# Kernel tuning notes

Hardware: AMD Instinct MI355X
Metric: run time of the kernel (lower is better)

The kernel has to match this reference:

```python
import jax, jax.numpy as jnp
import numpy as np

B, S, T = 512, 1024, 64


def setup_inputs() -> dict:
    key = jax.random.key(0)
    k1, k2, k3, k4, k5 = jax.random.split(key, 5)
    emissions = jax.random.normal(k1, (B, S, T), dtype=jnp.float32)
    tags = jax.random.randint(k2, (B, S), 0, T, dtype=jnp.int32)
    mask = jnp.ones((B, S), dtype=jnp.float32)
    start_transitions = jax.random.uniform(k3, (T,), minval=-0.1, maxval=0.1, dtype=jnp.float32)
    end_transitions = jax.random.uniform(k4, (T,), minval=-0.1, maxval=0.1, dtype=jnp.float32)
    transitions = jax.random.uniform(k5, (T, T), minval=-0.1, maxval=0.1, dtype=jnp.float32)
    return {"emissions": emissions, "mask": mask, "start_transitions": start_transitions,
            "end_transitions": end_transitions, "transitions": transitions, "tags": tags}


def _log_partition(emissions, mask, start_transitions, end_transitions, transitions):
    # forward-algorithm recurrence over time via lax.scan
    log_alpha0 = start_transitions + emissions[:, 0]  # [B, T]

    def step(log_alpha, xs):
        emit_t, mask_t = xs  # [B, T], [B]
        # [B, T_prev, T_next] -> logsumexp over previous tag
        score_t = log_alpha[:, :, None] + transitions[None, :, :] + emit_t[:, None, :]
        new_log_alpha = jax.nn.logsumexp(score_t, axis=1)
        log_alpha = jnp.where(mask_t[:, None] > 0, new_log_alpha, log_alpha)
        return log_alpha, None

    xs = (jnp.swapaxes(emissions[:, 1:], 0, 1), jnp.swapaxes(mask[:, 1:], 0, 1))
    log_alpha, _ = jax.lax.scan(step, log_alpha0, xs)
    log_alpha = log_alpha + end_transitions
    return jax.nn.logsumexp(log_alpha, axis=1).sum()


def _gold_score(emissions, tags, mask, start_transitions, end_transitions, transitions):
    tag0 = tags[:, 0]
    score = start_transitions[tag0] + jnp.take_along_axis(emissions[:, 0], tag0[:, None], axis=1)[:, 0]
    # vectorized over t = 1..S-1
    emit_t = jnp.take_along_axis(emissions[:, 1:], tags[:, 1:, None], axis=2)[..., 0]  # [B, S-1]
    trans_t = transitions[tags[:, :-1], tags[:, 1:]]  # [B, S-1]
    score = score + ((emit_t + trans_t) * mask[:, 1:]).sum(axis=1)
    last_idx = mask.sum(axis=1).astype(jnp.int32) - 1
    last_tags = jnp.take_along_axis(tags, last_idx[:, None], axis=1)[:, 0]
    score = score + end_transitions[last_tags]
    return score.sum()


def reference(emissions, mask, start_transitions, end_transitions, transitions, tags):
    log_den = _log_partition(emissions, mask, start_transitions, end_transitions, transitions)
    log_num = _gold_score(emissions, tags, mask, start_transitions, end_transitions, transitions)
    return log_num - log_den
```

## Files before the change

### kernel.cpp

```cpp
#include <hip/hip_runtime.h>

#define T64   64
#define SLEN  1024

typedef float f32x4  __attribute__((ext_vector_type(4)));
typedef short bf16x8 __attribute__((ext_vector_type(8)));

typedef const __attribute__((address_space(1))) void GV;
typedef __attribute__((address_space(3))) void LV;

static __device__ __forceinline__ short f2bf_rne(float f) {
  unsigned u = __builtin_bit_cast(unsigned, f);
  u += 0x7FFFu + ((u >> 16) & 1u);
  return (short)(u >> 16);
}
static __device__ __forceinline__ unsigned pkbf(float lo, float hi) {
  return __builtin_amdgcn_perm(__builtin_bit_cast(unsigned, hi),
                               __builtin_bit_cast(unsigned, lo), 0x07060302u);
}
static __device__ __forceinline__ bf16x8 packB(f32x4 a, f32x4 b) {
  union { unsigned u[4]; bf16x8 v; } r;
  r.u[0] = pkbf(a[0], a[1]); r.u[1] = pkbf(a[2], a[3]);
  r.u[2] = pkbf(b[0], b[1]); r.u[3] = pkbf(b[2], b[3]);
  return r.v;
}
static __device__ __forceinline__ f32x4 exp4(f32x4 x) {
  f32x4 r; r[0]=__expf(x[0]); r[1]=__expf(x[1]); r[2]=__expf(x[2]); r[3]=__expf(x[3]);
  return r;
}

#define MF(a, b, c) __builtin_amdgcn_mfma_f32_16x16x32_bf16((a), (b), (c), 0, 0, 0)

__global__ __launch_bounds__(64) void crf_scan(
    const float* __restrict__ em, const float* __restrict__ start_tr,
    const float* __restrict__ trans,
    float* __restrict__ wsF, float* __restrict__ accZ)
{
  __shared__ float ring[2 * 16 * 256];

  const int lane = threadIdx.x;
  const int g = lane >> 4, c = lane & 15;
  const unsigned cswz = (unsigned)((c & 7) << 4);
  const int h = blockIdx.x & 1;
  const int b = blockIdx.x >> 1;
  const float* embase = em + (size_t)b * (SLEN * T64);

  bf16x8 A00, A01, A10, A11, A20, A21, A30, A31;
#define FILLA(MT, KC, DST)                                                    \
  { bf16x8 a;                                                                 \
    _Pragma("unroll")                                                         \
    for (int e = 0; e < 8; ++e) {                                             \
      int to = 16 * (c >> 2) + 4 * (MT) + (c & 3);                            \
      int ti = 16 * g + 8 * (KC) + e;                                         \
      a[e] = f2bf_rne(__expf(trans[ti * T64 + to]));                          \
    }                                                                         \
    DST = a; }
  FILLA(0, 0, A00) FILLA(0, 1, A01) FILLA(1, 0, A10) FILLA(1, 1, A11)
  FILLA(2, 0, A20) FILLA(2, 1, A21) FILLA(3, 0, A30) FILLA(3, 1, A31)
#undef FILLA

  f32x4 e0q0 = {0,0,0,0}, e0q1 = {0,0,0,0}, e0q2 = {0,0,0,0}, e0q3 = {0,0,0,0};
  if (h == 0) {
    const float* r0 = embase + 16 * g;
    f32x4 v0 = *(const f32x4*)(r0 + 0),  v1 = *(const f32x4*)(r0 + 4);
    f32x4 v2 = *(const f32x4*)(r0 + 8),  v3 = *(const f32x4*)(r0 + 12);
#pragma unroll
    for (int r = 0; r < 4; ++r) {
      e0q0[r] = __expf(start_tr[16 * g + 0  + r] + v0[r]);
      e0q1[r] = __expf(start_tr[16 * g + 4  + r] + v1[r]);
      e0q2[r] = __expf(start_tr[16 * g + 8  + r] + v2[r]);
      e0q3[r] = __expf(start_tr[16 * g + 12 + r] + v3[r]);
    }
  }

  f32x4 q0 = {1,1,1,1}, q1 = {1,1,1,1}, q2 = {1,1,1,1}, q3 = {1,1,1,1};
  bf16x8 B0 = packB(q0, q1), B1 = packB(q2, q3);

#define ISSUE16(SSI, SLOT)                                                    \
  { _Pragma("unroll")                                                         \
    for (int cc = 0; cc < 16; ++cc) {                                         \
      int tc = 512 * h + 32 * cc - 8 + 4 * (SSI);                             \
      tc = tc < 0 ? 0 : tc;                                                   \
      int lp = (lane & 56) | ((lane ^ cc) & 7);                               \
      const float* src = embase + (size_t)tc * T64 + lp * 4;                  \
      __builtin_amdgcn_global_load_lds((GV*)src,                              \
          (LV*)&ring[(SLOT) * 4096 + cc * 256], 16, 0, 0);                    \
    } }

  ISSUE16(0, 0) ISSUE16(1, 1)

  const f32x4 zz = {0.f, 0.f, 0.f, 0.f};
  float ls = 0.0f;

  for (int ssi = 0; ssi < 10; ++ssi) {
    if (ssi == 9) { asm volatile("s_waitcnt vmcnt(0)"  ::: "memory"); }
    else          { asm volatile("s_waitcnt vmcnt(16)" ::: "memory"); }
    __builtin_amdgcn_sched_barrier(0);

    const char* sb = (const char*)ring + (ssi & 1) * 16384 + c * 1024;
    f32x4 E[4][4];
#pragma unroll
    for (int k = 0; k < 4; ++k)
#pragma unroll
      for (int mt = 0; mt < 4; ++mt)
        E[k][mt] = *(const f32x4*)(sb +
            (((unsigned)(k * 256 + g * 64 + 16 * mt)) ^ cswz));

#pragma unroll
    for (int k = 0; k < 4; ++k) {
      f32x4 d0 = MF(A00, B0, zz), d1 = MF(A10, B0, zz);
      f32x4 d2 = MF(A20, B0, zz), d3 = MF(A30, B0, zz);
      d0 = MF(A01, B1, d0); d1 = MF(A11, B1, d1);
      d2 = MF(A21, B1, d2); d3 = MF(A31, B1, d3);
      q0 = d0 * exp4(E[k][0]); q1 = d1 * exp4(E[k][1]);
      q2 = d2 * exp4(E[k][2]); q3 = d3 * exp4(E[k][3]);

      if (ssi == 2 && k == 0 && h == 0) {
        bool z = (c == 0);
        q0 = z ? e0q0 : q0; q1 = z ? e0q1 : q1;
        q2 = z ? e0q2 : q2; q3 = z ? e0q3 : q3;
      }

      if (k == 3 && (ssi & 1)) {
        float zt = ((q0[0]+q0[1])+(q0[2]+q0[3])) + ((q1[0]+q1[1])+(q1[2]+q1[3]))
                 + ((q2[0]+q2[1])+(q2[2]+q2[3])) + ((q3[0]+q3[1])+(q3[2]+q3[3]));
        zt += __shfl_xor(zt, 16, 64);
        zt += __shfl_xor(zt, 32, 64);
        float rz = __builtin_amdgcn_rcpf(zt);
        ls = (ssi == 1) ? 0.f : ls + __logf(zt);
        f32x4 rzv = {rz, rz, rz, rz};
        q0 *= rzv; q1 *= rzv; q2 *= rzv; q3 *= rzv;
      }
      B0 = packB(q0, q1); B1 = packB(q2, q3);
    }

    if (ssi + 2 < 10) {
      asm volatile("s_waitcnt lgkmcnt(0)" ::: "memory");
      __builtin_amdgcn_sched_barrier(0);
      ISSUE16(ssi + 2, (ssi & 1))
    }
  }
#undef ISSUE16

  if (h == 1 && c == 15) {
    *(f32x4*)(wsF + (size_t)b * T64 + 16 * g + 0)  = q0;
    *(f32x4*)(wsF + (size_t)b * T64 + 16 * g + 4)  = q1;
    *(f32x4*)(wsF + (size_t)b * T64 + 16 * g + 8)  = q2;
    *(f32x4*)(wsF + (size_t)b * T64 + 16 * g + 12) = q3;
  }
  ls += __shfl_xor(ls, 1, 64);
  ls += __shfl_xor(ls, 2, 64);
  ls += __shfl_xor(ls, 4, 64);
  ls += __shfl_xor(ls, 8, 64);
  if (lane == 0) atomicAdd(accZ, ls);
}

__global__ __launch_bounds__(64) void crf_gold(
    const float* __restrict__ em, const float* __restrict__ mask,
    const float* __restrict__ start_tr, const float* __restrict__ end_tr,
    const float* __restrict__ trans, const int* __restrict__ tags,
    float* __restrict__ accG)
{
  const int wid  = blockIdx.x;
  const int lane = threadIdx.x;
  const int*   tg = tags + (size_t)wid * SLEN;
  const float* mk = mask + (size_t)wid * SLEN;
  const float* eb = em + (size_t)wid * SLEN * T64;

  float part = 0.f, pm = 0.f;
  for (int it = 0; it < SLEN / 64; ++it) {
    int   t   = it * 64 + lane;
    int   tag = tg[t];
    float m   = mk[t];
    pm += m;
    if (t == 0) {
      part += start_tr[tag] + eb[tag];
    } else {
      int tp = tg[t - 1];
      part += (eb[(size_t)t * T64 + tag] + trans[tp * T64 + tag]) * m;
    }
  }
#pragma unroll
  for (int d = 1; d < 64; d <<= 1) pm += __shfl_xor(pm, d, 64);
#pragma unroll
  for (int d = 1; d < 64; d <<= 1) part += __shfl_xor(part, d, 64);
  if (lane == 0) {
    int last = (int)pm - 1;
    part += end_tr[tg[last]];
    atomicAdd(accG, part);
  }
}

__global__ void crf_combine(const float* __restrict__ wsF,
                            const float* __restrict__ end_tr,
                            float* __restrict__ accZ)
{
  const int wid  = (blockIdx.x * blockDim.x + threadIdx.x) >> 6;
  const int j    = threadIdx.x & 63;
  float v = wsF[(size_t)wid * T64 + j] * __expf(end_tr[j]);
#pragma unroll
  for (int d = 1; d < 64; d <<= 1) v += __shfl_xor(v, d, 64);
  if (j == 0) atomicAdd(accZ, __logf(v));
}

__global__ void crf_init(float* __restrict__ ws) { ws[0] = 0.f; ws[1] = 0.f; }

__global__ void crf_final(float* __restrict__ out, const float* __restrict__ ws)
{ out[0] = ws[0] - ws[1]; }

extern "C" void kernel_launch(void* const* d_in, const int* in_sizes, int n_in,
                              void* d_out, int out_size, void* d_ws, size_t ws_size,
                              hipStream_t stream)
{
  const float* em   = (const float*)d_in[0];
  const float* mask = (const float*)d_in[1];
  const float* st   = (const float*)d_in[2];
  const float* en   = (const float*)d_in[3];
  const float* tr   = (const float*)d_in[4];
  const int*   tags = (const int*)d_in[5];
  float* out = (float*)d_out;
  float* ws  = (float*)d_ws;

  const int B = in_sizes[1] / SLEN;

  float* accG = ws;
  float* accZ = ws + 1;
  float* wsF  = ws + 64;

  crf_init<<<1, 1, 0, stream>>>(ws);
  crf_scan<<<2 * B, 64, 0, stream>>>(em, st, tr, wsF, accZ);
  crf_gold<<<B, 64, 0, stream>>>(em, mask, st, en, tr, tags, accG);
  crf_combine<<<B / 4, 256, 0, stream>>>(wsF, en, accZ);
  crf_final<<<1, 1, 0, stream>>>(out, ws);
}
```

Measured before the change: 70.52 us.

## Fuse gold-path score into scan kernel reusing LDS-staged emissions

Removes the separate gold-score kernel. The scan kernel now stages tags and mask into LDS and picks the gold emission value from the emission tiles already sitting in the LDS ring, so emissions are not read a second time from global memory. The final-tag end transition and the mask sum move into the combine kernel. This adds LDS traffic, scalar work and a gather from the transition matrix to each scan step, and the launch grid is now a hardcoded block count.

```diff
diff --git a/kernel.cpp b/kernel.cpp
--- a/kernel.cpp
+++ b/kernel.cpp
@@ -2,6 +2,7 @@
 
 #define T64   64
 #define SLEN  1024
+#define NSCANB 1024
 
 typedef float f32x4  __attribute__((ext_vector_type(4)));
 typedef short bf16x8 __attribute__((ext_vector_type(8)));
@@ -31,12 +32,16 @@
 
 #define MF(a, b, c) __builtin_amdgcn_mfma_f32_16x16x32_bf16((a), (b), (c), 0, 0, 0)
 
-__global__ __launch_bounds__(64) void crf_scan(
-    const float* __restrict__ em, const float* __restrict__ start_tr,
-    const float* __restrict__ trans,
-    float* __restrict__ wsF, float* __restrict__ accZ)
+__global__ __launch_bounds__(64) void crf_fused(
+    const float* __restrict__ em, const float* __restrict__ mask,
+    const float* __restrict__ start_tr, const float* __restrict__ trans,
+    const int* __restrict__ tags,
+    float* __restrict__ wsF, float* __restrict__ accZ,
+    float* __restrict__ accG)
 {
   __shared__ float ring[2 * 16 * 256];
+  __shared__ int   tgl[513];
+  __shared__ float mkl[512];
 
   const int lane = threadIdx.x;
   const int g = lane >> 4, c = lane & 15;
@@ -44,6 +49,18 @@
   const int h = blockIdx.x & 1;
   const int b = blockIdx.x >> 1;
   const float* embase = em + (size_t)b * (SLEN * T64);
+
+  {
+    const int*   tgp = tags + (size_t)b * SLEN + 512 * h;
+    const float* mkp = mask + (size_t)b * SLEN + 512 * h;
+#pragma unroll
+    for (int it = 0; it < 8; ++it) {
+      int i = it * 64 + lane;
+      tgl[1 + i] = tgp[i];
+      mkl[i]     = mkp[i];
+    }
+    if (lane == 0) tgl[0] = h ? tgp[-1] : 0;
+  }
 
   bf16x8 A00, A01, A10, A11, A20, A21, A30, A31;
 #define FILLA(MT, KC, DST)                                                    \
@@ -90,7 +107,8 @@
   ISSUE16(0, 0) ISSUE16(1, 1)
 
   const f32x4 zz = {0.f, 0.f, 0.f, 0.f};
-  float ls = 0.0f;
+  float ls = 0.0f, gacc = 0.0f;
+  const int krow = lane >> 4, cl = lane & 15;
 
   for (int ssi = 0; ssi < 10; ++ssi) {
     if (ssi == 9) { asm volatile("s_waitcnt vmcnt(0)"  ::: "memory"); }
@@ -134,6 +152,23 @@
       B0 = packB(q0, q1); B1 = packB(q2, q3);
     }
 
+    {
+      int svar = 4 * ssi + krow;
+      if (svar >= 8) {
+        int ti  = 32 * cl + svar - 8;
+        int tag = tgl[1 + ti];
+        unsigned off = ((unsigned)(krow * 256 + tag * 4)) ^ ((unsigned)((cl & 7) << 4));
+        float ev = *(const float*)((const char*)ring +
+                      (ssi & 1) * 16384 + cl * 1024 + off);
+        if (h == 0 && ti == 0) {
+          gacc += start_tr[tag] + ev;
+        } else {
+          int tp = tgl[ti];
+          gacc += (ev + trans[tp * T64 + tag]) * mkl[ti];
+        }
+      }
+    }
+
     if (ssi + 2 < 10) {
       asm volatile("s_waitcnt lgkmcnt(0)" ::: "memory");
       __builtin_amdgcn_sched_barrier(0);
@@ -152,55 +187,38 @@
   ls += __shfl_xor(ls, 2, 64);
   ls += __shfl_xor(ls, 4, 64);
   ls += __shfl_xor(ls, 8, 64);
-  if (lane == 0) atomicAdd(accZ, ls);
-}
-
-__global__ __launch_bounds__(64) void crf_gold(
-    const float* __restrict__ em, const float* __restrict__ mask,
-    const float* __restrict__ start_tr, const float* __restrict__ end_tr,
-    const float* __restrict__ trans, const int* __restrict__ tags,
-    float* __restrict__ accG)
-{
-  const int wid  = blockIdx.x;
-  const int lane = threadIdx.x;
-  const int*   tg = tags + (size_t)wid * SLEN;
-  const float* mk = mask + (size_t)wid * SLEN;
-  const float* eb = em + (size_t)wid * SLEN * T64;
-
-  float part = 0.f, pm = 0.f;
-  for (int it = 0; it < SLEN / 64; ++it) {
-    int   t   = it * 64 + lane;
-    int   tag = tg[t];
-    float m   = mk[t];
-    pm += m;
-    if (t == 0) {
-      part += start_tr[tag] + eb[tag];
-    } else {
-      int tp = tg[t - 1];
-      part += (eb[(size_t)t * T64 + tag] + trans[tp * T64 + tag]) * m;
-    }
-  }
-#pragma unroll
-  for (int d = 1; d < 64; d <<= 1) pm += __shfl_xor(pm, d, 64);
-#pragma unroll
-  for (int d = 1; d < 64; d <<= 1) part += __shfl_xor(part, d, 64);
+#pragma unroll
+  for (int d = 1; d < 64; d <<= 1) gacc += __shfl_xor(gacc, d, 64);
   if (lane == 0) {
-    int last = (int)pm - 1;
-    part += end_tr[tg[last]];
-    atomicAdd(accG, part);
+    atomicAdd(accZ, ls);
+    atomicAdd(accG, gacc);
   }
 }
 
 __global__ void crf_combine(const float* __restrict__ wsF,
                             const float* __restrict__ end_tr,
-                            float* __restrict__ accZ)
+                            const float* __restrict__ mask,
+                            const int* __restrict__ tags,
+                            float* __restrict__ accZ,
+                            float* __restrict__ accG)
 {
   const int wid  = (blockIdx.x * blockDim.x + threadIdx.x) >> 6;
   const int j    = threadIdx.x & 63;
   float v = wsF[(size_t)wid * T64 + j] * __expf(end_tr[j]);
-#pragma unroll
-  for (int d = 1; d < 64; d <<= 1) v += __shfl_xor(v, d, 64);
-  if (j == 0) atomicAdd(accZ, __logf(v));
+  const float* mk = mask + (size_t)wid * SLEN;
+  float pm = 0.f;
+#pragma unroll
+  for (int it = 0; it < SLEN / 64; ++it) pm += mk[it * 64 + j];
+#pragma unroll
+  for (int d = 1; d < 64; d <<= 1) {
+    v  += __shfl_xor(v, d, 64);
+    pm += __shfl_xor(pm, d, 64);
+  }
+  if (j == 0) {
+    atomicAdd(accZ, __logf(v));
+    int last = (int)pm - 1;
+    atomicAdd(accG, end_tr[tags[(size_t)wid * SLEN + last]]);
+  }
 }
 
 __global__ void crf_init(float* __restrict__ ws) { ws[0] = 0.f; ws[1] = 0.f; }
@@ -228,8 +246,7 @@
   float* wsF  = ws + 64;
 
   crf_init<<<1, 1, 0, stream>>>(ws);
-  crf_scan<<<2 * B, 64, 0, stream>>>(em, st, tr, wsF, accZ);
-  crf_gold<<<B, 64, 0, stream>>>(em, mask, st, en, tr, tags, accG);
-  crf_combine<<<B / 4, 256, 0, stream>>>(wsF, en, accZ);
+  crf_fused<<<NSCANB, 64, 0, stream>>>(em, mask, st, tr, tags, wsF, accZ, accG);
+  crf_combine<<<B / 4, 256, 0, stream>>>(wsF, en, mask, tags, accZ, accG);
   crf_final<<<1, 1, 0, stream>>>(out, ws);
 }
```

Measured after the change: 75.57 us. 7.2% more time.
